# Kernel optimization log

Measured on AMD Instinct MI355X. Metric: run time of the kernel, lower is better.

The kernel has to match this reference:

```python
import jax, jax.numpy as jnp
import numpy as np
import math

D_MODEL, N_HEADS, D_FF = 1024, 16, 4096
HEAD_DIM = D_MODEL // N_HEADS
BATCH, SEQ = 2, 2048
POPE_BASE = 10000.0
LN_EPS = 1e-5


def setup_inputs() -> dict:
    key = jax.random.key(0)
    ks = jax.random.split(key, 20)
    s = 0.02
    inp = {
        "x": jax.random.normal(ks[0], (BATCH, SEQ, D_MODEL), dtype=jnp.float32),
        "positions": jnp.arange(SEQ, dtype=jnp.int64) if jax.config.jax_enable_x64 else jnp.arange(SEQ, dtype=jnp.int32),
        "Wq": jax.random.normal(ks[1], (D_MODEL, D_MODEL), jnp.float32) * s,
        "bq": jnp.zeros((D_MODEL,), jnp.float32),
        "Wk": jax.random.normal(ks[2], (D_MODEL, D_MODEL), jnp.float32) * s,
        "bk": jnp.zeros((D_MODEL,), jnp.float32),
        "Wv": jax.random.normal(ks[3], (D_MODEL, D_MODEL), jnp.float32) * s,
        "bv": jnp.zeros((D_MODEL,), jnp.float32),
        "Wo": jax.random.normal(ks[4], (D_MODEL, D_MODEL), jnp.float32) * s,
        "bo": jnp.zeros((D_MODEL,), jnp.float32),
        "phase_bias": jax.random.uniform(ks[5], (N_HEADS, HEAD_DIM), jnp.float32,
                                          minval=-2.0 * math.pi, maxval=0.0),
        "freqs": (1.0 / POPE_BASE ** (jnp.arange(HEAD_DIM, dtype=jnp.float32) / HEAD_DIM)),
        "W1": jax.random.normal(ks[6], (D_MODEL, D_FF), jnp.float32) * s,
        "b1": jnp.zeros((D_FF,), jnp.float32),
        "W2": jax.random.normal(ks[7], (D_FF, D_MODEL), jnp.float32) * s,
        "b2": jnp.zeros((D_MODEL,), jnp.float32),
        "g1": jnp.ones((D_MODEL,), jnp.float32),
        "beta1": jnp.zeros((D_MODEL,), jnp.float32),
        "g2": jnp.ones((D_MODEL,), jnp.float32),
        "beta2": jnp.zeros((D_MODEL,), jnp.float32),
    }
    return inp


def _layernorm(x, g, b):
    mu = jnp.mean(x, axis=-1, keepdims=True)
    var = jnp.mean((x - mu) ** 2, axis=-1, keepdims=True)
    return (x - mu) * jax.lax.rsqrt(var + LN_EPS) * g + b


def reference(x, positions, Wq, bq, Wk, bk, Wv, bv, Wo, bo, phase_bias, freqs,
              W1, b1, W2, b2, g1, beta1, g2, beta2):
    B, S, D = x.shape
    H, hd = N_HEADS, HEAD_DIM

    def split_heads(y):  # (B,S,D) -> (B,H,S,hd)
        return y.reshape(B, S, H, hd).transpose(0, 2, 1, 3)

    q = split_heads(x @ Wq + bq)
    k = split_heads(x @ Wk + bk)
    v = split_heads(x @ Wv + bv)

    # --- PoPE: magnitudes via softplus, phases from positions + learned bias ---
    mu_q = jax.nn.softplus(q)
    mu_k = jax.nn.softplus(k)
    pos_phases = positions[:, None].astype(jnp.float32) * freqs[None, :]        # (S,hd)
    phases = pos_phases[None, None, :, :] + phase_bias[None, :, None, :]        # (1,H,S,hd)
    cosp, sinp = jnp.cos(phases), jnp.sin(phases)
    q_pope = jnp.concatenate([mu_q * cosp, mu_q * sinp], axis=-1)               # (B,H,S,2hd)
    k_pope = jnp.concatenate([mu_k * cosp, mu_k * sinp], axis=-1)

    # --- manual causal attention with softmax1 ---
    scale = 1.0 / math.sqrt(2 * hd)  # q.shape[-1] == 2*head_dim under PoPE
    scores = jnp.einsum("bhsd,bhtd->bhst", q_pope, k_pope) * scale
    causal = jnp.triu(jnp.ones((S, S), dtype=bool), k=1)
    scores = jnp.where(causal[None, None], -jnp.inf, scores)
    m = jnp.max(scores, axis=-1, keepdims=True)
    e = jnp.exp(scores - m)
    attn_w = e / (1.0 + jnp.sum(e, axis=-1, keepdims=True))  # softmax1 (as written in source)
    attn = jnp.einsum("bhst,bhtd->bhsd", attn_w, v)

    attn = attn.transpose(0, 2, 1, 3).reshape(B, S, D) @ Wo + bo
    x = _layernorm(x + attn, g1, beta1)
    ff = jax.nn.relu(x @ W1 + b1) @ W2 + b2
    x = _layernorm(x + ff, g2, beta2)
    return x
```

## Files before the change

### kernel.cpp

```cpp
#include <hip/hip_runtime.h>
#include <hip/hip_bf16.h>
#include <math.h>

#define B_   2
#define S_   2048
#define D_   1024
#define H_   16
#define HD_  64
#define DFF_ 4096
#define M_   (B_*S_)
#define SCALE_ 0.08838834764831845f

typedef __attribute__((ext_vector_type(8))) short bf16x8;
typedef __attribute__((ext_vector_type(4))) float f32x4;

#define MFMA16(a,b,c) __builtin_amdgcn_mfma_f32_16x16x32_bf16((a),(b),(c),0,0,0)

__device__ __forceinline__ unsigned short f2b(float f) {
    union { float f; unsigned u; } v; v.f = f;
    return (unsigned short)((v.u + 0x7FFFu + ((v.u >> 16) & 1u)) >> 16);
}
__device__ __forceinline__ float b2f(unsigned short s) {
    union { unsigned u; float f; } v; v.u = ((unsigned)s) << 16;
    return v.f;
}
__device__ __forceinline__ unsigned pk2bf(float a, float b) {
    union { float f; unsigned u; } ua, ub; ua.f = a; ub.f = b;
    return __builtin_amdgcn_perm(ub.u, ua.u, 0x07060302u);
}
__device__ __forceinline__ float softplus_f(float x) {
    return fmaxf(x, 0.f) + log1pf(__expf(-fabsf(x)));
}
__device__ __forceinline__ void g2l16(const void* g, void* l) {
    __builtin_amdgcn_global_load_lds(
        (const __attribute__((address_space(1))) unsigned int*)g,
        (__attribute__((address_space(3))) unsigned int*)l, 16, 0, 0);
}

__global__ __launch_bounds__(256) void conv_bf16_kernel(
    const float* __restrict__ in, unsigned short* __restrict__ out)
{
    int i = (blockIdx.x * 256 + threadIdx.x) * 4;
    float4 v = *(const float4*)&in[i];
    ushort4 o;
    o.x = f2b(v.x); o.y = f2b(v.y); o.z = f2b(v.z); o.w = f2b(v.w);
    *(ushort4*)&out[i] = o;
}

__global__ __launch_bounds__(256) void wtrans_kernel(
    const float* __restrict__ W, unsigned short* __restrict__ WT, int K, int N)
{
    __shared__ float tile[32][33];
    const int n0 = blockIdx.x * 32, k0 = blockIdx.y * 32;
    const int tx = threadIdx.x & 31, ty = threadIdx.x >> 5;
    #pragma unroll
    for (int i = 0; i < 4; i++)
        tile[ty + 8*i][tx] = W[(size_t)(k0 + ty + 8*i) * N + n0 + tx];
    __syncthreads();
    #pragma unroll
    for (int i = 0; i < 4; i++)
        WT[(size_t)(n0 + ty + 8*i) * K + k0 + tx] = f2b(tile[tx][ty + 8*i]);
}

__global__ __launch_bounds__(256) void bcat_kernel(
    const float* __restrict__ a, const float* __restrict__ b,
    const float* __restrict__ c, float* __restrict__ o)
{
    int i = blockIdx.x * 256 + threadIdx.x;
    o[i] = (i < 1024) ? a[i] : (i < 2048 ? b[i - 1024] : c[i - 2048]);
}

__global__ __launch_bounds__(256) void gemm_bf16_kernel(
    const unsigned short* __restrict__ A,
    const unsigned short* __restrict__ WT,
    const float* __restrict__ bias,
    float* __restrict__ outF, unsigned short* __restrict__ outB,
    int M, int Kslice, int lda, int N, int relu)
{
    __shared__ unsigned short As[2][128 * 64];
    __shared__ unsigned short Bs[2][128 * 64];

    const int tid = threadIdx.x;
    const int w = tid >> 6, lane = tid & 63;
    const int quad = lane >> 4, l16 = lane & 15;

    const int nn = gridDim.x, nm = gridDim.y;
    const int lin = ((int)blockIdx.z * nm + (int)blockIdx.y) * nn + (int)blockIdx.x;
    const int per = (nn * nm * (int)gridDim.z) >> 3;
    const int id  = (lin & 7) * per + (lin >> 3);
    const int zz  = id / (nn * nm);
    const int rem = id - zz * nn * nm;
    const int mt_ = rem / nn, nt_ = rem - mt_ * nn;

    const size_t m0 = (size_t)mt_ * 128, n0 = (size_t)nt_ * 128;
    const int wm = (w >> 1) * 64, wn = (w & 1) * 64;
    const int koff = zz * Kslice;

    const int srow = lane >> 3;
    const int sc   = ((lane & 7) ^ srow) * 8;
    const unsigned short* ga = A  + (m0 + w * 32 + srow) * (size_t)lda + koff + sc;
    const unsigned short* gb = WT + (n0 + w * 32 + srow) * (size_t)lda + koff + sc;
    const size_t rows8 = (size_t)8 * lda;

    f32x4 acc[4][4] = {};
    const int niter = Kslice >> 6;

    #pragma unroll
    for (int j = 0; j < 4; j++) g2l16(ga + j * rows8, &As[0][(w * 32 + j * 8) * 64]);
    #pragma unroll
    for (int j = 0; j < 4; j++) g2l16(gb + j * rows8, &Bs[0][(w * 32 + j * 8) * 64]);

    for (int i = 0; i < niter; i++) {
        __syncthreads();
        if (i + 1 < niter) {
            const int nb = (i + 1) & 1, k0 = (i + 1) << 6;
            #pragma unroll
            for (int j = 0; j < 4; j++)
                g2l16(ga + j * rows8 + k0, &As[nb][(w * 32 + j * 8) * 64]);
            #pragma unroll
            for (int j = 0; j < 4; j++)
                g2l16(gb + j * rows8 + k0, &Bs[nb][(w * 32 + j * 8) * 64]);
        }
        const int buf = i & 1;

        #pragma unroll
        for (int kk = 0; kk < 2; kk++) {
            bf16x8 af[4], bfr[4];
            #pragma unroll
            for (int t = 0; t < 4; t++) {
                const int slot = ((kk * 4 + quad) ^ (l16 & 7)) * 8;
                af[t]  = *(const bf16x8*)&As[buf][(wm + t * 16 + l16) * 64 + slot];
                bfr[t] = *(const bf16x8*)&Bs[buf][(wn + t * 16 + l16) * 64 + slot];
            }
            #pragma unroll
            for (int mt = 0; mt < 4; mt++)
                #pragma unroll
                for (int nt = 0; nt < 4; nt++)
                    acc[mt][nt] = MFMA16(af[mt], bfr[nt], acc[mt][nt]);
        }
    }

    float bv[4];
    #pragma unroll
    for (int nt = 0; nt < 4; nt++)
        bv[nt] = (zz == 0) ? bias[n0 + wn + nt * 16 + l16] : 0.f;

    float* outFz = outF ? outF + (size_t)zz * M * N : nullptr;

    #pragma unroll
    for (int mt = 0; mt < 4; mt++) {
        #pragma unroll
        for (int nt = 0; nt < 4; nt++) {
            const size_t n = n0 + wn + nt * 16 + l16;
            #pragma unroll
            for (int r = 0; r < 4; r++) {
                const size_t m = m0 + wm + mt * 16 + quad * 4 + r;
                float val = acc[mt][nt][r] + bv[nt];
                if (relu) val = fmaxf(val, 0.f);
                const size_t idx = m * N + n;
                if (outFz) outFz[idx] = val;
                if (outB) outB[idx] = f2b(val);
            }
        }
    }
}

__global__ __launch_bounds__(256) void pope_kernel(
    const unsigned short* __restrict__ qkv,
    const float* __restrict__ phase_bias, const float* __restrict__ freqs,
    unsigned short* __restrict__ qp, unsigned short* __restrict__ kp)
{
    int idx = blockIdx.x * 256 + threadIdx.x;
    int d = idx & 63;
    int s = (idx >> 6) & (S_ - 1);
    int h = (idx >> 17) & (H_ - 1);
    int b = idx >> 21;

    size_t src = (size_t)(b * S_ + s) * 3072 + h * HD_ + d;
    float muq = softplus_f(b2f(qkv[src])) * SCALE_;
    float muk = softplus_f(b2f(qkv[src + 1024]));

    float ph = (float)s * freqs[d] + phase_bias[h * HD_ + d];
    float sn, cs;
    sincosf(ph, &sn, &cs);

    size_t o = ((size_t)(b * H_ + h) * S_ + s) * 128 + d;
    qp[o]      = f2b(muq * cs);
    qp[o + 64] = f2b(muq * sn);
    kp[o]      = f2b(muk * cs);
    kp[o + 64] = f2b(muk * sn);
}

__global__ __launch_bounds__(256) void vtrans_kernel(
    const unsigned short* __restrict__ qkv, unsigned short* __restrict__ vt)
{
    __shared__ unsigned short tile[64][72];
    const int bh = blockIdx.y, b = bh >> 4, h = bh & 15;
    const int s0 = blockIdx.x * 64;
    const int tid = threadIdx.x;
    #pragma unroll
    for (int i = 0; i < 16; i++) {
        int idx = i * 256 + tid;
        int s = idx >> 6, d = idx & 63;
        tile[s][d] = qkv[(size_t)(b * S_ + s0 + s) * 3072 + 2048 + h * HD_ + d];
    }
    __syncthreads();
    #pragma unroll
    for (int i = 0; i < 16; i++) {
        int idx = i * 256 + tid;
        int d = idx >> 6, s = idx & 63;
        vt[((size_t)bh * 64 + d) * S_ + s0 + s] = tile[s][d];
    }
}

__global__ __launch_bounds__(512, 4) void attn_mfma_kernel(
    const unsigned short* __restrict__ qp,
    const unsigned short* __restrict__ kp,
    const unsigned short* __restrict__ vt,
    unsigned short* __restrict__ ao)
{
    __shared__ unsigned short kt_lds[2][64][128];
    __shared__ unsigned short vt_lds[2][64][64];
    __shared__ unsigned short p_lds[8][16][72];

    const int tid = threadIdx.x;
    const int w = tid >> 6, lane = tid & 63;
    const int quad = lane >> 4, l16 = lane & 15;
    const int bh = blockIdx.y, b = bh >> 4, h = bh & 15;

    const int a = (blockIdx.z == 0) ? 15 - (int)blockIdx.x : (int)blockIdx.x;
    const int q0b = a * 128;
    const int q0 = q0b + w * 16;

    const unsigned short* qbase = qp + ((size_t)bh * S_ + q0 + l16) * 128 + quad * 8;
    bf16x8 qa[4];
    #pragma unroll
    for (int kc = 0; kc < 4; kc++) qa[kc] = *(const bf16x8*)(qbase + kc * 32);

    const int krow = lane >> 4, kslot = lane & 15;
    const int vrow = lane >> 3, vslot = lane & 7;
    const int kr0 = w * 8 + krow,     kc0 = kslot ^ (kr0 & 15);
    const int kr1 = w * 8 + 4 + krow, kc1 = kslot ^ (kr1 & 15);
    const int vd  = w * 8 + vrow,     vc  = vslot ^ (vd & 7);
    const unsigned short* kg0 = kp + ((size_t)bh * S_ + kr0) * 128 + kc0 * 8;
    const unsigned short* kg1 = kp + ((size_t)bh * S_ + kr1) * 128 + kc1 * 8;
    const unsigned short* vg0 = vt + ((size_t)bh * 64 + vd) * S_ + vc * 8;

    f32x4 o[4] = {};
    float ms = -1e30f, ls = 0.f;

    const int ntiles = 2 * a + 2;

    g2l16(kg0, &kt_lds[0][w * 8][0]);
    g2l16(kg1, &kt_lds[0][w * 8 + 4][0]);
    g2l16(vg0, &vt_lds[0][w * 8][0]);

    for (int ti = 0; ti < ntiles; ti++) {
        const int t0 = ti * 64;
        __syncthreads();
        if (ti + 1 < ntiles) {
            const int nb = (ti + 1) & 1;
            const size_t ko = (size_t)(ti + 1) * (64 * 128);
            const size_t vo = (size_t)(ti + 1) * 64;
            g2l16(kg0 + ko, &kt_lds[nb][w * 8][0]);
            g2l16(kg1 + ko, &kt_lds[nb][w * 8 + 4][0]);
            g2l16(vg0 + vo, &vt_lds[nb][w * 8][0]);
        }
        const int buf = ti & 1;

        if (t0 <= q0 + 15) {
            f32x4 sf[4];
            #pragma unroll
            for (int kg = 0; kg < 4; kg++) {
                f32x4 s = {0, 0, 0, 0};
                const int row = kg * 16 + l16;
                #pragma unroll
                for (int kc = 0; kc < 4; kc++) {
                    const int slot = (kc * 4 + quad) ^ l16;
                    s = MFMA16(*(const bf16x8*)&kt_lds[buf][row][slot * 8], qa[kc], s);
                }
                sf[kg] = s;
            }

            const int qrow = q0 + l16;
            const bool dmask = (t0 + 63 > q0);
            #pragma unroll
            for (int kg = 0; kg < 4; kg++) {
                const int kbase = t0 + kg * 16 + quad * 4;
                float v0 = sf[kg][0], v1 = sf[kg][1], v2 = sf[kg][2], v3 = sf[kg][3];
                if (dmask) {
                    v0 = (kbase     <= qrow) ? v0 : -1e30f;
                    v1 = (kbase + 1 <= qrow) ? v1 : -1e30f;
                    v2 = (kbase + 2 <= qrow) ? v2 : -1e30f;
                    v3 = (kbase + 3 <= qrow) ? v3 : -1e30f;
                }
                ms = fmaxf(ms, fmaxf(fmaxf(v0, v1), fmaxf(v2, v3)));
                const float e0 = __expf(v0), e1 = __expf(v1);
                const float e2 = __expf(v2), e3 = __expf(v3);
                ls += (e0 + e1) + (e2 + e3);
                uint2 pk;
                pk.x = pk2bf(e0, e1);
                pk.y = pk2bf(e2, e3);
                *(uint2*)&p_lds[w][l16][kg * 16 + quad * 4] = pk;
            }
            asm volatile("s_waitcnt lgkmcnt(0)" ::: "memory");
            bf16x8 pa0 = *(const bf16x8*)&p_lds[w][l16][quad * 8];
            bf16x8 pa1 = *(const bf16x8*)&p_lds[w][l16][quad * 8 + 32];

            #pragma unroll
            for (int dg = 0; dg < 4; dg++) {
                const int row = dg * 16 + l16;
                const int s0_ = quad ^ (l16 & 7);
                const int s1_ = (quad + 4) ^ (l16 & 7);
                o[dg] = MFMA16(pa0, *(const bf16x8*)&vt_lds[buf][row][s0_ * 8], o[dg]);
                o[dg] = MFMA16(pa1, *(const bf16x8*)&vt_lds[buf][row][s1_ * 8], o[dg]);
            }
        }
    }

    float mv = ms, lv = ls;
    mv = fmaxf(mv, __shfl_xor(mv, 16, 64)); lv += __shfl_xor(lv, 16, 64);
    mv = fmaxf(mv, __shfl_xor(mv, 32, 64)); lv += __shfl_xor(lv, 32, 64);
    const float inv = 1.f / (__expf(mv) + lv);

    #pragma unroll
    for (int r = 0; r < 4; r++) {
        const float ir = __shfl(inv, quad * 4 + r, 64);
        const int row = q0 + quad * 4 + r;
        const size_t base = (size_t)(b * S_ + row) * D_ + h * HD_ + l16;
        ao[base]      = f2b(o[0][r] * ir);
        ao[base + 16] = f2b(o[1][r] * ir);
        ao[base + 32] = f2b(o[2][r] * ir);
        ao[base + 48] = f2b(o[3][r] * ir);
    }
}

__global__ __launch_bounds__(256) void ln_kernel(
    const float* __restrict__ ya, const float* __restrict__ yb,
    const float* __restrict__ resF, const unsigned short* __restrict__ resB,
    const float* __restrict__ g, const float* __restrict__ beta,
    float* __restrict__ outF, unsigned short* __restrict__ outB)
{
    const int row = blockIdx.x;
    const int tid = threadIdx.x;
    const float* yr = ya + (size_t)row * D_;
    const float* y2 = yb ? yb + (size_t)row * D_ : nullptr;

    float t[4];
    float sum = 0.f, sumsq = 0.f;
    #pragma unroll
    for (int i = 0; i < 4; i++) {
        int c = tid + 256 * i;
        float rv = resF ? resF[(size_t)row * D_ + c] : b2f(resB[(size_t)row * D_ + c]);
        t[i] = yr[c] + rv + (y2 ? y2[c] : 0.f);
        sum += t[i]; sumsq += t[i] * t[i];
    }
    #pragma unroll
    for (int off = 32; off >= 1; off >>= 1) {
        sum   += __shfl_xor(sum,   off, 64);
        sumsq += __shfl_xor(sumsq, off, 64);
    }
    __shared__ float rs_[4], rq_[4];
    int w = tid >> 6, lane = tid & 63;
    if (lane == 0) { rs_[w] = sum; rq_[w] = sumsq; }
    __syncthreads();
    float tot  = rs_[0] + rs_[1] + rs_[2] + rs_[3];
    float totq = rq_[0] + rq_[1] + rq_[2] + rq_[3];
    float mu   = tot  * (1.f / D_);
    float var  = totq * (1.f / D_) - mu * mu;
    float rstd = rsqrtf(var + 1e-5f);

    #pragma unroll
    for (int i = 0; i < 4; i++) {
        int c = tid + 256 * i;
        float val = (t[i] - mu) * rstd * g[c] + beta[c];
        if (outF) outF[(size_t)row * D_ + c] = val;
        if (outB) outB[(size_t)row * D_ + c] = f2b(val);
    }
}

extern "C" void kernel_launch(void* const* d_in, const int* in_sizes, int n_in,
                              void* d_out, int out_size, void* d_ws, size_t ws_size,
                              hipStream_t stream)
{
    const float* x   = (const float*)d_in[0];
    const float* Wq  = (const float*)d_in[2];
    const float* bq  = (const float*)d_in[3];
    const float* Wk  = (const float*)d_in[4];
    const float* bk  = (const float*)d_in[5];
    const float* Wv  = (const float*)d_in[6];
    const float* bv  = (const float*)d_in[7];
    const float* Wo  = (const float*)d_in[8];
    const float* bo  = (const float*)d_in[9];
    const float* phase_bias = (const float*)d_in[10];
    const float* freqs = (const float*)d_in[11];
    const float* W1  = (const float*)d_in[12];
    const float* b1  = (const float*)d_in[13];
    const float* W2  = (const float*)d_in[14];
    const float* b2  = (const float*)d_in[15];
    const float* g1  = (const float*)d_in[16];
    const float* be1 = (const float*)d_in[17];
    const float* g2  = (const float*)d_in[18];
    const float* be2 = (const float*)d_in[19];
    float* out = (float*)d_out;

    char* base = (char*)d_ws;
    const size_t MiB = 1024 * 1024;
    unsigned short* WqkvT = (unsigned short*)(base);
    unsigned short* WoT   = (unsigned short*)(base + 6  * MiB);
    unsigned short* W1T   = (unsigned short*)(base + 8  * MiB);
    unsigned short* W2T   = (unsigned short*)(base + 16 * MiB);
    float*          bqkv  = (float*)(base + 24 * MiB);
    unsigned short* xb    = (unsigned short*)(base + 25 * MiB);
    unsigned short* qkvb  = (unsigned short*)(base + 33 * MiB);
    unsigned short* qpb   = (unsigned short*)(base + 57 * MiB);
    unsigned short* kpb   = (unsigned short*)(base + 73 * MiB);
    unsigned short* vtb   = (unsigned short*)(base + 89 * MiB);
    float*          po    = (float*)(base + 89 * MiB);
    unsigned short* aob   = xb;
    unsigned short* x1b   = xb;
    unsigned short* hb    = qkvb;
    float*          fo    = po;

    dim3 blk(256);

    conv_bf16_kernel<<<dim3(M_ * D_ / 1024), blk, 0, stream>>>(x, xb);
    wtrans_kernel<<<dim3(32, 32), blk, 0, stream>>>(Wq, WqkvT, D_, D_);
    wtrans_kernel<<<dim3(32, 32), blk, 0, stream>>>(Wk, WqkvT + (size_t)1024 * 1024, D_, D_);
    wtrans_kernel<<<dim3(32, 32), blk, 0, stream>>>(Wv, WqkvT + (size_t)2048 * 1024, D_, D_);
    wtrans_kernel<<<dim3(32, 32), blk, 0, stream>>>(Wo, WoT, D_, D_);
    wtrans_kernel<<<dim3(DFF_ / 32, D_ / 32), blk, 0, stream>>>(W1, W1T, D_, DFF_);
    wtrans_kernel<<<dim3(D_ / 32, DFF_ / 32), blk, 0, stream>>>(W2, W2T, DFF_, D_);
    bcat_kernel<<<dim3(12), blk, 0, stream>>>(bq, bk, bv, bqkv);

    gemm_bf16_kernel<<<dim3(3072 / 128, M_ / 128, 1), blk, 0, stream>>>(
        xb, WqkvT, bqkv, nullptr, qkvb, M_, D_, D_, 3072, 0);

    pope_kernel<<<dim3(B_ * H_ * S_ * HD_ / 256), blk, 0, stream>>>(
        qkvb, phase_bias, freqs, qpb, kpb);
    vtrans_kernel<<<dim3(S_ / 64, B_ * H_), blk, 0, stream>>>(qkvb, vtb);

    attn_mfma_kernel<<<dim3(8, B_ * H_, 2), dim3(512), 0, stream>>>(qpb, kpb, vtb, aob);

    gemm_bf16_kernel<<<dim3(D_ / 128, M_ / 128, 2), blk, 0, stream>>>(
        aob, WoT, bo, po, nullptr, M_, D_ / 2, D_, D_, 0);
    ln_kernel<<<dim3(M_), blk, 0, stream>>>(
        po, po + (size_t)M_ * D_, x, nullptr, g1, be1, nullptr, x1b);

    gemm_bf16_kernel<<<dim3(DFF_ / 128, M_ / 128, 1), blk, 0, stream>>>(
        x1b, W1T, b1, nullptr, hb, M_, D_, D_, DFF_, 1);
    gemm_bf16_kernel<<<dim3(D_ / 128, M_ / 128, 2), blk, 0, stream>>>(
        hb, W2T, b2, fo, nullptr, M_, DFF_ / 2, DFF_, D_, 0);
    ln_kernel<<<dim3(M_), blk, 0, stream>>>(
        fo, fo + (size_t)M_ * D_, nullptr, x1b, g2, be2, out, nullptr);
}
```

Before: 401.3 us.

## Add 256x256-tile 8-wave GEMM with interleaved LDS staging for QKV and FFN1

Adds a 512-thread GEMM kernel with 256x256 output tiles, double-buffered LDS, and a four-phase schedule. Each phase interleaves LDS fragment reads, async global-to-LDS staging and MFMA blocks, with priority raised around the MFMA blocks. It also uses an XCD-aware block remap, and the QKV and W1 projections now run on it. Separately, the four square weight transposes are merged into one launch. The larger tiles aim to raise arithmetic intensity and overlap loads with compute, at the cost of fewer blocks (192 and 256) and heavy register and LDS use.

```diff
diff --git a/kernel.cpp b/kernel.cpp
--- a/kernel.cpp
+++ b/kernel.cpp
@@ -60,6 +60,26 @@
     #pragma unroll
     for (int i = 0; i < 4; i++)
         WT[(size_t)(n0 + ty + 8*i) * K + k0 + tx] = f2b(tile[tx][ty + 8*i]);
+}
+
+__global__ __launch_bounds__(256) void wtrans4_kernel(
+    const float* __restrict__ Wa, const float* __restrict__ Wb,
+    const float* __restrict__ Wc, const float* __restrict__ Wd,
+    unsigned short* __restrict__ Tabc, unsigned short* __restrict__ Td)
+{
+    __shared__ float tile[32][33];
+    const int z = blockIdx.z;
+    const float* W = (z == 0) ? Wa : (z == 1) ? Wb : (z == 2) ? Wc : Wd;
+    unsigned short* WT = (z < 3) ? Tabc + (size_t)z * 1024 * 1024 : Td;
+    const int n0 = blockIdx.x * 32, k0 = blockIdx.y * 32;
+    const int tx = threadIdx.x & 31, ty = threadIdx.x >> 5;
+    #pragma unroll
+    for (int i = 0; i < 4; i++)
+        tile[ty + 8*i][tx] = W[(size_t)(k0 + ty + 8*i) * 1024 + n0 + tx];
+    __syncthreads();
+    #pragma unroll
+    for (int i = 0; i < 4; i++)
+        WT[(size_t)(n0 + ty + 8*i) * 1024 + k0 + tx] = f2b(tile[tx][ty + 8*i]);
 }
 
 __global__ __launch_bounds__(256) void bcat_kernel(
@@ -163,6 +183,172 @@
             }
         }
     }
+}
+
+__global__ __launch_bounds__(512, 2) void gemm256_bf16_kernel(
+    const unsigned short* __restrict__ A,
+    const unsigned short* __restrict__ WT,
+    const float* __restrict__ bias,
+    float* __restrict__ outF, unsigned short* __restrict__ outB,
+    int M, int Kslice, int lda, int N, int relu)
+{
+    __shared__ unsigned short As[2][256 * 64];
+    __shared__ unsigned short Bs[2][256 * 64];
+
+    const int tid = threadIdx.x;
+    const int w = tid >> 6, lane = tid & 63;
+    const int quad = lane >> 4, l16 = lane & 15;
+    const int wm_ = w >> 2, wn_ = w & 3;
+
+    const int nn = gridDim.x, nm = gridDim.y;
+    const int lin = ((int)blockIdx.z * nm + (int)blockIdx.y) * nn + (int)blockIdx.x;
+    const int per = (nn * nm * (int)gridDim.z) >> 3;
+    const int id  = (lin & 7) * per + (lin >> 3);
+    const int zz  = id / (nn * nm);
+    const int rem = id - zz * nn * nm;
+    const int mt_ = rem / nn, nt_ = rem - mt_ * nn;
+
+    const size_t m0 = (size_t)mt_ * 256, n0 = (size_t)nt_ * 256;
+    const int koff = zz * Kslice;
+
+    const int srow = lane >> 3;
+    const int sc   = ((lane & 7) ^ srow) * 8;
+    const unsigned short* ga = A  + (m0 + w * 8 + srow) * (size_t)lda + koff + sc;
+    const unsigned short* gb = WT + (n0 + w * 8 + srow) * (size_t)lda + koff + sc;
+    const size_t rows64    = (size_t)64 * lda;
+    const size_t half_rows = (size_t)128 * lda;
+
+    const int s0 = (quad ^ (l16 & 7)) * 8;
+    const int s1 = s0 ^ 32;
+
+    const int niter = Kslice >> 6;
+
+#define STAGE_A(BUF, T, H) do { \
+    const size_t k0_ = (size_t)(T) << 6; \
+    g2l16(ga + (size_t)(H) * half_rows + k0_,          &As[BUF][((H) * 128 + w * 8) * 64]); \
+    g2l16(ga + (size_t)(H) * half_rows + rows64 + k0_, &As[BUF][((H) * 128 + 64 + w * 8) * 64]); \
+} while (0)
+
+#define STAGE_B(BUF, T, H) do { \
+    const size_t k0_ = (size_t)(T) << 6; \
+    g2l16(gb + (size_t)(H) * half_rows + k0_,          &Bs[BUF][((H) * 128 + w * 8) * 64]); \
+    g2l16(gb + (size_t)(H) * half_rows + rows64 + k0_, &Bs[BUF][((H) * 128 + 64 + w * 8) * 64]); \
+} while (0)
+
+#define RD_A(DST, BUF, MROW, KK) \
+    DST = *(const bf16x8*)&As[BUF][(wm_ * 128 + (MROW) * 16 + l16) * 64 + ((KK) ? s1 : s0)]
+#define RD_B(DST, BUF, NROW, KK) \
+    DST = *(const bf16x8*)&Bs[BUF][(wn_ * 64 + (NROW) * 16 + l16) * 64 + ((KK) ? s1 : s0)]
+
+#define MM8(MOFF, NOFF, AR, BR) do { \
+    _Pragma("unroll") \
+    for (int kk_ = 0; kk_ < 2; ++kk_) { \
+        _Pragma("unroll") \
+        for (int mf_ = 0; mf_ < 4; ++mf_) { \
+            _Pragma("unroll") \
+            for (int nf_ = 0; nf_ < 2; ++nf_) \
+                acc[(MOFF) + mf_][(NOFF) + nf_] = \
+                    MFMA16(AR[mf_][kk_], BR[nf_][kk_], acc[(MOFF) + mf_][(NOFF) + nf_]); \
+        } \
+    } \
+} while (0)
+
+    f32x4 acc[8][4] = {};
+    bf16x8 a_lo[4][2], b_lo[2][2];
+    bf16x8 a_hi[4][2] = {};
+    bf16x8 b_hi[2][2] = {};
+
+    STAGE_B(0, 0, 0); STAGE_B(0, 0, 1);
+    STAGE_A(0, 0, 0); STAGE_A(0, 0, 1);
+    STAGE_B(1, 1, 0); STAGE_B(1, 1, 1);
+    asm volatile("s_waitcnt vmcnt(4)" ::: "memory");
+    __builtin_amdgcn_s_barrier();
+
+#define PERIOD(BUF, T) do { \
+    const int t_ = (T); \
+     \
+    RD_A(a_lo[0][0], BUF, 0, 0); RD_A(a_lo[0][1], BUF, 0, 1); \
+    RD_A(a_lo[1][0], BUF, 1, 0); RD_A(a_lo[1][1], BUF, 1, 1); \
+    RD_A(a_lo[2][0], BUF, 2, 0); RD_A(a_lo[2][1], BUF, 2, 1); \
+    RD_A(a_lo[3][0], BUF, 3, 0); RD_A(a_lo[3][1], BUF, 3, 1); \
+    RD_B(b_lo[0][0], BUF, 0, 0); RD_B(b_lo[0][1], BUF, 0, 1); \
+    RD_B(b_lo[1][0], BUF, 1, 0); RD_B(b_lo[1][1], BUF, 1, 1); \
+    if (t_ + 1 < niter) STAGE_A((BUF) ^ 1, t_ + 1, 0); \
+    __builtin_amdgcn_s_barrier(); \
+    asm volatile("s_waitcnt lgkmcnt(0)" ::: "memory"); \
+    __builtin_amdgcn_s_setprio(1); \
+    MM8(4, 2, a_hi, b_hi); \
+    __builtin_amdgcn_s_setprio(0); \
+    __builtin_amdgcn_s_barrier(); \
+     \
+    RD_B(b_hi[0][0], BUF, 2, 0); RD_B(b_hi[0][1], BUF, 2, 1); \
+    RD_B(b_hi[1][0], BUF, 3, 0); RD_B(b_hi[1][1], BUF, 3, 1); \
+    if (t_ + 1 < niter) STAGE_A((BUF) ^ 1, t_ + 1, 1); \
+    __builtin_amdgcn_s_barrier(); \
+    asm volatile("s_waitcnt lgkmcnt(0)" ::: "memory"); \
+    __builtin_amdgcn_s_setprio(1); \
+    MM8(0, 0, a_lo, b_lo); \
+    __builtin_amdgcn_s_setprio(0); \
+    __builtin_amdgcn_s_barrier(); \
+     \
+    RD_A(a_hi[0][0], BUF, 4, 0); RD_A(a_hi[0][1], BUF, 4, 1); \
+    RD_A(a_hi[1][0], BUF, 5, 0); RD_A(a_hi[1][1], BUF, 5, 1); \
+    RD_A(a_hi[2][0], BUF, 6, 0); RD_A(a_hi[2][1], BUF, 6, 1); \
+    RD_A(a_hi[3][0], BUF, 7, 0); RD_A(a_hi[3][1], BUF, 7, 1); \
+    if (t_ + 2 < niter) STAGE_B(BUF, t_ + 2, 0); \
+    __builtin_amdgcn_s_barrier(); \
+    asm volatile("s_waitcnt lgkmcnt(0)" ::: "memory"); \
+    __builtin_amdgcn_s_setprio(1); \
+    MM8(0, 2, a_lo, b_hi); \
+    __builtin_amdgcn_s_setprio(0); \
+    __builtin_amdgcn_s_barrier(); \
+     \
+    if (t_ + 2 < niter) STAGE_B(BUF, t_ + 2, 1); \
+    __builtin_amdgcn_s_barrier(); \
+    __builtin_amdgcn_s_setprio(1); \
+    MM8(4, 0, a_hi, b_lo); \
+    __builtin_amdgcn_s_setprio(0); \
+    if (t_ + 2 < niter) { asm volatile("s_waitcnt vmcnt(4)" ::: "memory"); } \
+    else                { asm volatile("s_waitcnt vmcnt(0)" ::: "memory"); } \
+    __builtin_amdgcn_s_barrier(); \
+} while (0)
+
+    for (int t = 0; t < niter; t += 2) {
+        PERIOD(0, t);
+        PERIOD(1, t + 1);
+    }
+    MM8(4, 2, a_hi, b_hi);
+
+    float bv[4];
+    #pragma unroll
+    for (int nf = 0; nf < 4; nf++)
+        bv[nf] = (zz == 0) ? bias[n0 + wn_ * 64 + nf * 16 + l16] : 0.f;
+
+    float* outFz = outF ? outF + (size_t)zz * M * N : nullptr;
+
+    #pragma unroll
+    for (int mf = 0; mf < 8; mf++) {
+        #pragma unroll
+        for (int nf = 0; nf < 4; nf++) {
+            const size_t n = n0 + wn_ * 64 + nf * 16 + l16;
+            #pragma unroll
+            for (int r = 0; r < 4; r++) {
+                const size_t m = m0 + wm_ * 128 + mf * 16 + quad * 4 + r;
+                float val = acc[mf][nf][r] + bv[nf];
+                if (relu) val = fmaxf(val, 0.f);
+                const size_t idx = m * N + n;
+                if (outFz) outFz[idx] = val;
+                if (outB) outB[idx] = f2b(val);
+            }
+        }
+    }
+
+#undef STAGE_A
+#undef STAGE_B
+#undef RD_A
+#undef RD_B
+#undef MM8
+#undef PERIOD
 }
 
 __global__ __launch_bounds__(256) void pope_kernel(
@@ -425,15 +611,12 @@
     dim3 blk(256);
 
     conv_bf16_kernel<<<dim3(M_ * D_ / 1024), blk, 0, stream>>>(x, xb);
-    wtrans_kernel<<<dim3(32, 32), blk, 0, stream>>>(Wq, WqkvT, D_, D_);
-    wtrans_kernel<<<dim3(32, 32), blk, 0, stream>>>(Wk, WqkvT + (size_t)1024 * 1024, D_, D_);
-    wtrans_kernel<<<dim3(32, 32), blk, 0, stream>>>(Wv, WqkvT + (size_t)2048 * 1024, D_, D_);
-    wtrans_kernel<<<dim3(32, 32), blk, 0, stream>>>(Wo, WoT, D_, D_);
+    wtrans4_kernel<<<dim3(32, 32, 4), blk, 0, stream>>>(Wq, Wk, Wv, Wo, WqkvT, WoT);
     wtrans_kernel<<<dim3(DFF_ / 32, D_ / 32), blk, 0, stream>>>(W1, W1T, D_, DFF_);
     wtrans_kernel<<<dim3(D_ / 32, DFF_ / 32), blk, 0, stream>>>(W2, W2T, DFF_, D_);
     bcat_kernel<<<dim3(12), blk, 0, stream>>>(bq, bk, bv, bqkv);
 
-    gemm_bf16_kernel<<<dim3(3072 / 128, M_ / 128, 1), blk, 0, stream>>>(
+    gemm256_bf16_kernel<<<dim3(3072 / 256, M_ / 256, 1), dim3(512), 0, stream>>>(
         xb, WqkvT, bqkv, nullptr, qkvb, M_, D_, D_, 3072, 0);
 
     pope_kernel<<<dim3(B_ * H_ * S_ * HD_ / 256), blk, 0, stream>>>(
@@ -447,7 +630,7 @@
     ln_kernel<<<dim3(M_), blk, 0, stream>>>(
         po, po + (size_t)M_ * D_, x, nullptr, g1, be1, nullptr, x1b);
 
-    gemm_bf16_kernel<<<dim3(DFF_ / 128, M_ / 128, 1), blk, 0, stream>>>(
+    gemm256_bf16_kernel<<<dim3(DFF_ / 256, M_ / 256, 1), dim3(512), 0, stream>>>(
         x1b, W1T, b1, nullptr, hb, M_, D_, D_, DFF_, 1);
     gemm_bf16_kernel<<<dim3(D_ / 128, M_ / 128, 2), blk, 0, stream>>>(
         hb, W2T, b2, fo, nullptr, M_, DFF_ / 2, DFF_, D_, 0);
```

New measurement: 418.6 us. 4.3% more time.

## Fuse PoPE into QKV GEMM epilogue, batch weight transposes, add MFMA priority hints

Applied to the files above, without the earlier changes.

The QKV GEMM now applies bias, softplus, sin/cos phase rotation and scaling in its epilogue and writes the PoPE-expanded Q and K directly. This removes the separate pope kernel and its round trip of Q/K through global memory, and only V goes to the intermediate buffer. The four square weight transposes are merged into one launch, and the bias concat is folded into the input conversion kernel. s_setprio hints are wrapped around the attention MFMA sections. The trade-off is a heavier epilogue, with per-element sincos and scattered 2-byte stores that coalesce poorly in the fused kernel.

```diff
diff --git a/kernel.cpp b/kernel.cpp
--- a/kernel.cpp
+++ b/kernel.cpp
@@ -38,13 +38,18 @@
 }
 
 __global__ __launch_bounds__(256) void conv_bf16_kernel(
-    const float* __restrict__ in, unsigned short* __restrict__ out)
+    const float* __restrict__ in, unsigned short* __restrict__ out,
+    const float* __restrict__ bq, const float* __restrict__ bk,
+    const float* __restrict__ bv, float* __restrict__ bqkv)
 {
     int i = (blockIdx.x * 256 + threadIdx.x) * 4;
     float4 v = *(const float4*)&in[i];
     ushort4 o;
     o.x = f2b(v.x); o.y = f2b(v.y); o.z = f2b(v.z); o.w = f2b(v.w);
     *(ushort4*)&out[i] = o;
+    int j = blockIdx.x * 256 + threadIdx.x;
+    if (j < 3072)
+        bqkv[j] = (j < 1024) ? bq[j] : (j < 2048 ? bk[j - 1024] : bv[j - 2048]);
 }
 
 __global__ __launch_bounds__(256) void wtrans_kernel(
@@ -62,12 +67,24 @@
         WT[(size_t)(n0 + ty + 8*i) * K + k0 + tx] = f2b(tile[tx][ty + 8*i]);
 }
 
-__global__ __launch_bounds__(256) void bcat_kernel(
-    const float* __restrict__ a, const float* __restrict__ b,
-    const float* __restrict__ c, float* __restrict__ o)
-{
-    int i = blockIdx.x * 256 + threadIdx.x;
-    o[i] = (i < 1024) ? a[i] : (i < 2048 ? b[i - 1024] : c[i - 2048]);
+__global__ __launch_bounds__(256) void wtrans4_kernel(
+    const float* __restrict__ Wa, const float* __restrict__ Wb,
+    const float* __restrict__ Wc, const float* __restrict__ Wd,
+    unsigned short* __restrict__ Tabc, unsigned short* __restrict__ Td)
+{
+    __shared__ float tile[32][33];
+    const int z = blockIdx.z;
+    const float* W = (z == 0) ? Wa : (z == 1) ? Wb : (z == 2) ? Wc : Wd;
+    unsigned short* WT = (z < 3) ? Tabc + (size_t)z * 1024 * 1024 : Td;
+    const int n0 = blockIdx.x * 32, k0 = blockIdx.y * 32;
+    const int tx = threadIdx.x & 31, ty = threadIdx.x >> 5;
+    #pragma unroll
+    for (int i = 0; i < 4; i++)
+        tile[ty + 8*i][tx] = W[(size_t)(k0 + ty + 8*i) * 1024 + n0 + tx];
+    __syncthreads();
+    #pragma unroll
+    for (int i = 0; i < 4; i++)
+        WT[(size_t)(n0 + ty + 8*i) * 1024 + k0 + tx] = f2b(tile[tx][ty + 8*i]);
 }
 
 __global__ __launch_bounds__(256) void gemm_bf16_kernel(
@@ -165,30 +182,118 @@
     }
 }
 
-__global__ __launch_bounds__(256) void pope_kernel(
-    const unsigned short* __restrict__ qkv,
+__global__ __launch_bounds__(256) void gemm_qkv_pope_kernel(
+    const unsigned short* __restrict__ A,
+    const unsigned short* __restrict__ WT,
+    const float* __restrict__ bias,
     const float* __restrict__ phase_bias, const float* __restrict__ freqs,
-    unsigned short* __restrict__ qp, unsigned short* __restrict__ kp)
-{
-    int idx = blockIdx.x * 256 + threadIdx.x;
-    int d = idx & 63;
-    int s = (idx >> 6) & (S_ - 1);
-    int h = (idx >> 17) & (H_ - 1);
-    int b = idx >> 21;
-
-    size_t src = (size_t)(b * S_ + s) * 3072 + h * HD_ + d;
-    float muq = softplus_f(b2f(qkv[src])) * SCALE_;
-    float muk = softplus_f(b2f(qkv[src + 1024]));
-
-    float ph = (float)s * freqs[d] + phase_bias[h * HD_ + d];
-    float sn, cs;
-    sincosf(ph, &sn, &cs);
-
-    size_t o = ((size_t)(b * H_ + h) * S_ + s) * 128 + d;
-    qp[o]      = f2b(muq * cs);
-    qp[o + 64] = f2b(muq * sn);
-    kp[o]      = f2b(muk * cs);
-    kp[o + 64] = f2b(muk * sn);
+    unsigned short* __restrict__ qp, unsigned short* __restrict__ kp,
+    unsigned short* __restrict__ vb)
+{
+    __shared__ unsigned short As[2][128 * 64];
+    __shared__ unsigned short Bs[2][128 * 64];
+
+    const int tid = threadIdx.x;
+    const int w = tid >> 6, lane = tid & 63;
+    const int quad = lane >> 4, l16 = lane & 15;
+
+    const int nn = gridDim.x, nm = gridDim.y;
+    const int lin = (int)blockIdx.y * nn + (int)blockIdx.x;
+    const int per = (nn * nm) >> 3;
+    const int id  = (lin & 7) * per + (lin >> 3);
+    const int mt_ = id / nn, nt_ = id - mt_ * nn;
+
+    const size_t m0 = (size_t)mt_ * 128, n0 = (size_t)nt_ * 128;
+    const int wm = (w >> 1) * 64, wn = (w & 1) * 64;
+
+    const int srow = lane >> 3;
+    const int sc   = ((lane & 7) ^ srow) * 8;
+    const unsigned short* ga = A  + (m0 + w * 32 + srow) * (size_t)D_ + sc;
+    const unsigned short* gb = WT + (n0 + w * 32 + srow) * (size_t)D_ + sc;
+    const size_t rows8 = (size_t)8 * D_;
+
+    f32x4 acc[4][4] = {};
+    const int niter = D_ >> 6;
+
+    #pragma unroll
+    for (int j = 0; j < 4; j++) g2l16(ga + j * rows8, &As[0][(w * 32 + j * 8) * 64]);
+    #pragma unroll
+    for (int j = 0; j < 4; j++) g2l16(gb + j * rows8, &Bs[0][(w * 32 + j * 8) * 64]);
+
+    for (int i = 0; i < niter; i++) {
+        __syncthreads();
+        if (i + 1 < niter) {
+            const int nb = (i + 1) & 1, k0 = (i + 1) << 6;
+            #pragma unroll
+            for (int j = 0; j < 4; j++)
+                g2l16(ga + j * rows8 + k0, &As[nb][(w * 32 + j * 8) * 64]);
+            #pragma unroll
+            for (int j = 0; j < 4; j++)
+                g2l16(gb + j * rows8 + k0, &Bs[nb][(w * 32 + j * 8) * 64]);
+        }
+        const int buf = i & 1;
+
+        #pragma unroll
+        for (int kk = 0; kk < 2; kk++) {
+            bf16x8 af[4], bfr[4];
+            #pragma unroll
+            for (int t = 0; t < 4; t++) {
+                const int slot = ((kk * 4 + quad) ^ (l16 & 7)) * 8;
+                af[t]  = *(const bf16x8*)&As[buf][(wm + t * 16 + l16) * 64 + slot];
+                bfr[t] = *(const bf16x8*)&Bs[buf][(wn + t * 16 + l16) * 64 + slot];
+            }
+            #pragma unroll
+            for (int mt = 0; mt < 4; mt++)
+                #pragma unroll
+                for (int nt = 0; nt < 4; nt++)
+                    acc[mt][nt] = MFMA16(af[mt], bfr[nt], acc[mt][nt]);
+        }
+    }
+
+    const int isQ = (n0 < 1024), isV = (n0 >= 2048);
+
+    if (isV) {
+        #pragma unroll
+        for (int mt = 0; mt < 4; mt++) {
+            #pragma unroll
+            for (int nt = 0; nt < 4; nt++) {
+                const size_t n = n0 + wn + nt * 16 + l16;
+                const float bn = bias[n];
+                #pragma unroll
+                for (int r = 0; r < 4; r++) {
+                    const size_t m = m0 + wm + mt * 16 + quad * 4 + r;
+                    vb[m * 3072 + n] = f2b(acc[mt][nt][r] + bn);
+                }
+            }
+        }
+    } else {
+        unsigned short* dst = isQ ? qp : kp;
+        #pragma unroll
+        for (int nt = 0; nt < 4; nt++) {
+            const int n  = (int)n0 + wn + nt * 16 + l16;
+            const int nq = isQ ? n : n - 1024;
+            const int h  = nq >> 6, d = nq & 63;
+            const float fr = freqs[d];
+            const float pb = phase_bias[h * 64 + d];
+            const float bn = bias[n];
+            #pragma unroll
+            for (int mt = 0; mt < 4; mt++) {
+                #pragma unroll
+                for (int r = 0; r < 4; r++) {
+                    const int m = (int)m0 + wm + mt * 16 + quad * 4 + r;
+                    const int s = m & (S_ - 1), b = m >> 11;
+                    float mu = softplus_f(acc[mt][nt][r] + bn);
+                    if (isQ) mu *= SCALE_;
+                    float ph = (float)s * fr + pb;
+                    float sn, cs;
+                    sincosf(ph, &sn, &cs);
+                    const size_t o = ((size_t)(b * H_ + h) * S_ + s) * 128 + d;
+                    dst[o]      = f2b(mu * cs);
+                    dst[o + 64] = f2b(mu * sn);
+                }
+            }
+        }
+    }
 }
 
 __global__ __launch_bounds__(256) void vtrans_kernel(
@@ -270,6 +375,7 @@
 
         if (t0 <= q0 + 15) {
             f32x4 sf[4];
+            __builtin_amdgcn_s_setprio(1);
             #pragma unroll
             for (int kg = 0; kg < 4; kg++) {
                 f32x4 s = {0, 0, 0, 0};
@@ -281,6 +387,7 @@
                 }
                 sf[kg] = s;
             }
+            __builtin_amdgcn_s_setprio(0);
 
             const int qrow = q0 + l16;
             const bool dmask = (t0 + 63 > q0);
@@ -307,6 +414,7 @@
             bf16x8 pa0 = *(const bf16x8*)&p_lds[w][l16][quad * 8];
             bf16x8 pa1 = *(const bf16x8*)&p_lds[w][l16][quad * 8 + 32];
 
+            __builtin_amdgcn_s_setprio(1);
             #pragma unroll
             for (int dg = 0; dg < 4; dg++) {
                 const int row = dg * 16 + l16;
@@ -315,6 +423,7 @@
                 o[dg] = MFMA16(pa0, *(const bf16x8*)&vt_lds[buf][row][s0_ * 8], o[dg]);
                 o[dg] = MFMA16(pa1, *(const bf16x8*)&vt_lds[buf][row][s1_ * 8], o[dg]);
             }
+            __builtin_amdgcn_s_setprio(0);
         }
     }
 
@@ -424,20 +533,14 @@
 
     dim3 blk(256);
 
-    conv_bf16_kernel<<<dim3(M_ * D_ / 1024), blk, 0, stream>>>(x, xb);
-    wtrans_kernel<<<dim3(32, 32), blk, 0, stream>>>(Wq, WqkvT, D_, D_);
-    wtrans_kernel<<<dim3(32, 32), blk, 0, stream>>>(Wk, WqkvT + (size_t)1024 * 1024, D_, D_);
-    wtrans_kernel<<<dim3(32, 32), blk, 0, stream>>>(Wv, WqkvT + (size_t)2048 * 1024, D_, D_);
-    wtrans_kernel<<<dim3(32, 32), blk, 0, stream>>>(Wo, WoT, D_, D_);
+    conv_bf16_kernel<<<dim3(M_ * D_ / 1024), blk, 0, stream>>>(x, xb, bq, bk, bv, bqkv);
+    wtrans4_kernel<<<dim3(32, 32, 4), blk, 0, stream>>>(Wq, Wk, Wv, Wo, WqkvT, WoT);
     wtrans_kernel<<<dim3(DFF_ / 32, D_ / 32), blk, 0, stream>>>(W1, W1T, D_, DFF_);
     wtrans_kernel<<<dim3(D_ / 32, DFF_ / 32), blk, 0, stream>>>(W2, W2T, DFF_, D_);
-    bcat_kernel<<<dim3(12), blk, 0, stream>>>(bq, bk, bv, bqkv);
-
-    gemm_bf16_kernel<<<dim3(3072 / 128, M_ / 128, 1), blk, 0, stream>>>(
-        xb, WqkvT, bqkv, nullptr, qkvb, M_, D_, D_, 3072, 0);
-
-    pope_kernel<<<dim3(B_ * H_ * S_ * HD_ / 256), blk, 0, stream>>>(
-        qkvb, phase_bias, freqs, qpb, kpb);
+
+    gemm_qkv_pope_kernel<<<dim3(3072 / 128, M_ / 128, 1), blk, 0, stream>>>(
+        xb, WqkvT, bqkv, phase_bias, freqs, qpb, kpb, qkvb);
+
     vtrans_kernel<<<dim3(S_ / 64, B_ * H_), blk, 0, stream>>>(qkvb, vtb);
 
     attn_mfma_kernel<<<dim3(8, B_ * H_, 2), dim3(512), 0, stream>>>(qpb, kpb, vtb, aob);
```

Result: slower. 742.9 us (+85.1%).
